# Optimization experiments

Hardware: AMD Instinct MI355X
Metric: run time of the kernel (lower is better)

## Reference

```python
import jax, jax.numpy as jnp
import numpy as np

R = 131072          # total proposals (ROIs)
D = 1024            # input feature dim (ShapeSpec.channels)
NUM_CLASSES = 80    # COCO foreground classes
REID_DIM = 256      # reid_feat_dim
BOX_DIM = 4


def setup_inputs() -> dict:
    key = jax.random.key(0)
    ks = jax.random.split(key, 12)
    x = jax.random.normal(ks[0], (R, D), dtype=jnp.float32)
    # cls_score: Linear(D, num_classes+1), init std=0.01, bias 0
    W_cls = 0.01 * jax.random.normal(ks[1], (NUM_CLASSES + 1, D), dtype=jnp.float32)
    b_cls = jnp.zeros((NUM_CLASSES + 1,), dtype=jnp.float32)
    # bbox_pred: Linear(D, num_classes * 4), init std=0.001, bias 0
    W_bbox = 0.001 * jax.random.normal(ks[2], (NUM_CLASSES * BOX_DIM, D), dtype=jnp.float32)
    b_bbox = jnp.zeros((NUM_CLASSES * BOX_DIM,), dtype=jnp.float32)
    # reid_embed_head: MLP(D, 256, 256, 3) -> Linear(D,256), Linear(256,256), Linear(256,256)
    def lin(k, fan_in, fan_out):
        kw, kb = jax.random.split(k)
        bound = 1.0 / np.sqrt(fan_in)
        W = jax.random.uniform(kw, (fan_out, fan_in), minval=-bound, maxval=bound, dtype=jnp.float32)
        b = jax.random.uniform(kb, (fan_out,), minval=-bound, maxval=bound, dtype=jnp.float32)
        return W, b
    W1, b1 = lin(ks[3], D, REID_DIM)
    W2, b2 = lin(ks[4], REID_DIM, REID_DIM)
    W3, b3 = lin(ks[5], REID_DIM, REID_DIM)
    return {"x": x, "W_cls": W_cls, "b_cls": b_cls, "W_bbox": W_bbox, "b_bbox": b_bbox,
            "W1": W1, "b1": b1, "W2": W2, "b2": b2, "W3": W3, "b3": b3}


def reference(x, W_cls, b_cls, W_bbox, b_bbox, W1, b1, W2, b2, W3, b3):
    # x: [R, D] (already flat; torch forward flattens if dim > 2)
    scores = x @ W_cls.T + b_cls                 # [R, K+1]
    proposal_deltas = x @ W_bbox.T + b_bbox      # [R, K*4]
    # MLP with ReLU on all but last layer
    h = jax.nn.relu(x @ W1.T + b1)               # [R, 256]
    h = jax.nn.relu(h @ W2.T + b2)               # [R, 256]
    embeds = h @ W3.T + b3                       # [R, 256]
    return scores, proposal_deltas, embeds
```

## Files before the change

### kernel.cpp

```cpp
#include <hip/hip_runtime.h>
#include <hip/hip_bf16.h>
#include <stdint.h>

#define R_TOT   131072
#define D_IN    1024
#define N_CLS   81
#define N_BOX   320
#define N_H     256
#define N1_USED 657
#define N1_PAD  672
#define NB_COLS 336

typedef __attribute__((ext_vector_type(8))) short short8;
typedef __attribute__((ext_vector_type(4))) float f32x4;

__device__ __forceinline__ unsigned short f2bf(float f) {
  union { float f; unsigned u; } v; v.f = f;
  unsigned r = v.u + 0x7FFFu + ((v.u >> 16) & 1u);
  return (unsigned short)(r >> 16);
}

__device__ __forceinline__ short8 cvt8(float4 a, float4 b) {
  short8 v;
  v[0] = (short)f2bf(a.x); v[1] = (short)f2bf(a.y);
  v[2] = (short)f2bf(a.z); v[3] = (short)f2bf(a.w);
  v[4] = (short)f2bf(b.x); v[5] = (short)f2bf(b.y);
  v[6] = (short)f2bf(b.z); v[7] = (short)f2bf(b.w);
  return v;
}

__device__ __forceinline__ void async_lds16(void* lds, const void* g) {
  __builtin_amdgcn_global_load_lds(
      (const __attribute__((address_space(1))) unsigned int*)g,
      (__attribute__((address_space(3))) unsigned int*)lds, 16, 0, 0);
}

__global__ void prep_w1(const float* __restrict__ Wc, const float* __restrict__ Wb,
                        const float* __restrict__ W1, unsigned short* __restrict__ Wp)
{
  int idx = blockIdx.x * 256 + threadIdx.x;
  int p   = idx / (N1_PAD * 32);
  int rem = idx % (N1_PAD * 32);
  int n   = rem >> 5;
  int kk  = rem & 31;
  int k   = p * 32 + kk;
  float w = 0.f;
  if (n < N_CLS)               w = Wc[(size_t)n * D_IN + k];
  else if (n < N_CLS + N_BOX)  w = Wb[(size_t)(n - N_CLS) * D_IN + k];
  else if (n < N1_USED)        w = W1[(size_t)(n - (N_CLS + N_BOX)) * D_IN + k];
  Wp[idx] = f2bf(w);
}

__global__ void prep_w23(const float* __restrict__ W2, const float* __restrict__ W3,
                         unsigned short* __restrict__ W2b, unsigned short* __restrict__ W3b)
{
  int idx = blockIdx.x * 256 + threadIdx.x;
  if (idx < 65536) W2b[idx] = f2bf(W2[idx]);
  else             W3b[idx - 65536] = f2bf(W3[idx - 65536]);
}

__global__ __launch_bounds__(448) void g1_kernel(
    const float* __restrict__ x, const unsigned short* __restrict__ Wp,
    const float* __restrict__ b_cls, const float* __restrict__ b_box,
    const float* __restrict__ b1,
    float* __restrict__ scores, float* __restrict__ deltas,
    unsigned short* __restrict__ h1)
{
  __shared__ __attribute__((aligned(16))) unsigned short As[2][64 * 32];

  const int tid  = threadIdx.x;
  const int wave = tid >> 6;
  const int lane = tid & 63;
  const int orig  = blockIdx.x;
  const int work  = (orig & 7) * 512 + (orig >> 3);
  const int m0    = (work >> 1) * 64;
  const int nbase = (work & 1) * NB_COLS;

  const int arow = tid >> 2;
  const int akq  = tid & 3;
  const int awoff = arow * 32 + ((akq ^ ((arow >> 1) & 3)) << 3);

  const int lr = lane & 15;
  const int g2 = (lane >> 4) * 8;

  f32x4 acc[4][3];
#pragma unroll
  for (int i = 0; i < 4; ++i)
#pragma unroll
    for (int j = 0; j < 3; ++j)
      acc[i][j] = (f32x4){0.f, 0.f, 0.f, 0.f};

  const unsigned short* bptr = Wp + (size_t)(nbase + wave * 48 + lr) * 32 + g2;
  const size_t BSTEP = (size_t)N1_PAD * 32;

  if (tid < 256) {
    const float* s = x + (size_t)(m0 + arow) * D_IN + akq * 8;
    float4 f0 = *(const float4*)s;
    float4 f1 = *(const float4*)(s + 4);
    *(short8*)&As[0][awoff] = cvt8(f0, f1);
  }
  short8 bCur0 = *(const short8*)(bptr);
  short8 bCur1 = *(const short8*)(bptr + 512);
  short8 bCur2 = *(const short8*)(bptr + 1024);
  bptr += BSTEP;
  asm volatile("s_waitcnt lgkmcnt(0)" ::: "memory");
  __builtin_amdgcn_sched_barrier(0);
  __builtin_amdgcn_s_barrier();

#pragma unroll 2
  for (int kp = 0; kp < 32; ++kp) {
    const int cur = kp & 1;

    float4 f0, f1;
    if (kp < 31 && tid < 256) {
      const float* s = x + (size_t)(m0 + arow) * D_IN + (size_t)(kp + 1) * 32 + akq * 8;
      f0 = *(const float4*)s;
      f1 = *(const float4*)(s + 4);
    }
    short8 bn0, bn1, bn2;
    if (kp < 31) {
      bn0 = *(const short8*)(bptr);
      bn1 = *(const short8*)(bptr + 512);
      bn2 = *(const short8*)(bptr + 1024);
      bptr += BSTEP;
    }

#pragma unroll
    for (int mi = 0; mi < 4; ++mi) {
      const int r  = mi * 16 + lr;
      const int sl = (g2 >> 3) ^ ((r >> 1) & 3);
      short8 af = *(const short8*)&As[cur][r * 32 + (sl << 3)];
      acc[mi][0] = __builtin_amdgcn_mfma_f32_16x16x32_bf16(af, bCur0, acc[mi][0], 0, 0, 0);
      acc[mi][1] = __builtin_amdgcn_mfma_f32_16x16x32_bf16(af, bCur1, acc[mi][1], 0, 0, 0);
      acc[mi][2] = __builtin_amdgcn_mfma_f32_16x16x32_bf16(af, bCur2, acc[mi][2], 0, 0, 0);
    }

    if (kp < 31 && tid < 256)
      *(short8*)&As[cur ^ 1][awoff] = cvt8(f0, f1);

    if (kp < 31) { bCur0 = bn0; bCur1 = bn1; bCur2 = bn2; }

    asm volatile("s_waitcnt lgkmcnt(0)" ::: "memory");
    __builtin_amdgcn_sched_barrier(0);
    __builtin_amdgcn_s_barrier();
  }

  const int rbase = m0 + ((lane >> 4) << 2);
#pragma unroll
  for (int mi = 0; mi < 4; ++mi) {
#pragma unroll
    for (int ni = 0; ni < 3; ++ni) {
      int n = nbase + wave * 48 + ni * 16 + lr;
      if (n >= N1_USED) continue;
      if (n < N_CLS) {
        float bb = b_cls[n];
#pragma unroll
        for (int j = 0; j < 4; ++j) {
          int r = rbase + mi * 16 + j;
          scores[(size_t)r * N_CLS + n] = acc[mi][ni][j] + bb;
        }
      } else if (n < N_CLS + N_BOX) {
        int nb = n - N_CLS;
        float bb = b_box[nb];
#pragma unroll
        for (int j = 0; j < 4; ++j) {
          int r = rbase + mi * 16 + j;
          deltas[(size_t)r * N_BOX + nb] = acc[mi][ni][j] + bb;
        }
      } else {
        int nh = n - (N_CLS + N_BOX);
        float bb = b1[nh];
#pragma unroll
        for (int j = 0; j < 4; ++j) {
          int r = rbase + mi * 16 + j;
          float h = acc[mi][ni][j] + bb;
          h1[(size_t)r * N_H + nh] = f2bf(fmaxf(h, 0.f));
        }
      }
    }
  }
}

__device__ __forceinline__ void g23_stage(unsigned short* Asb, unsigned short* Bsb,
    const unsigned short* __restrict__ A, const unsigned short* __restrict__ Bw,
    int m0, int kp, int tid)
{
  {
    int row = tid >> 2, kq = tid & 3;
    async_lds16((char*)Asb + tid * 16,
                (const char*)(A + (size_t)(m0 + row) * N_H + (size_t)kp * 32 + kq * 8));
  }
#pragma unroll
  for (int i = 0; i < 2; ++i) {
    int chunk = tid + i * 512;
    int row = chunk >> 2, kq = chunk & 3;
    async_lds16((char*)Bsb + chunk * 16,
                (const char*)(Bw + (size_t)row * N_H + (size_t)kp * 32 + kq * 8));
  }
}

template <int RELU, int OUT_BF16>
__global__ __launch_bounds__(512, 1) void g23_kernel(
    const unsigned short* __restrict__ A, const unsigned short* __restrict__ Bw,
    const float* __restrict__ bias, void* __restrict__ outv)
{
  __shared__ __attribute__((aligned(16))) unsigned short As[2][128 * 32];
  __shared__ __attribute__((aligned(16))) unsigned short Bs[2][256 * 32];
  const int tid  = threadIdx.x;
  const int wave = tid >> 6, lane = tid & 63;
  const int wm = wave >> 2, wn = wave & 3;
  const int m0 = blockIdx.x * 128;

  f32x4 acc[4][4];
#pragma unroll
  for (int i = 0; i < 4; ++i)
#pragma unroll
    for (int j = 0; j < 4; ++j)
      acc[i][j] = (f32x4){0.f, 0.f, 0.f, 0.f};

  g23_stage(&As[0][0], &Bs[0][0], A, Bw, m0, 0, tid);
  __syncthreads();

  const int lr = lane & 15;
  const int lk = (lane >> 4) * 8;

  for (int kp = 0; kp < 8; ++kp) {
    const int cur = kp & 1, nxt = cur ^ 1;
    if (kp < 7) g23_stage(&As[nxt][0], &Bs[nxt][0], A, Bw, m0, kp + 1, tid);

    short8 af[4], bfr[4];
#pragma unroll
    for (int mi = 0; mi < 4; ++mi)
      af[mi] = *(const short8*)&As[cur][(wm * 64 + mi * 16 + lr) * 32 + lk];
#pragma unroll
    for (int ni = 0; ni < 4; ++ni)
      bfr[ni] = *(const short8*)&Bs[cur][(wn * 64 + ni * 16 + lr) * 32 + lk];
#pragma unroll
    for (int mi = 0; mi < 4; ++mi)
#pragma unroll
      for (int ni = 0; ni < 4; ++ni)
        acc[mi][ni] = __builtin_amdgcn_mfma_f32_16x16x32_bf16(af[mi], bfr[ni], acc[mi][ni], 0, 0, 0);
    __syncthreads();
  }

#pragma unroll
  for (int mi = 0; mi < 4; ++mi) {
#pragma unroll
    for (int ni = 0; ni < 4; ++ni) {
      int n = wn * 64 + ni * 16 + lr;
      float bb = bias[n];
#pragma unroll
      for (int j = 0; j < 4; ++j) {
        int r = m0 + wm * 64 + mi * 16 + ((lane >> 4) << 2) + j;
        float v = acc[mi][ni][j] + bb;
        if (RELU) v = fmaxf(v, 0.f);
        if (OUT_BF16) ((unsigned short*)outv)[(size_t)r * N_H + n] = f2bf(v);
        else          ((float*)outv)[(size_t)r * N_H + n] = v;
      }
    }
  }
}

extern "C" void kernel_launch(void* const* d_in, const int* in_sizes, int n_in,
                              void* d_out, int out_size, void* d_ws, size_t ws_size,
                              hipStream_t stream)
{
  const float* x     = (const float*)d_in[0];
  const float* W_cls = (const float*)d_in[1];
  const float* b_cls = (const float*)d_in[2];
  const float* W_box = (const float*)d_in[3];
  const float* b_box = (const float*)d_in[4];
  const float* W1    = (const float*)d_in[5];
  const float* b1    = (const float*)d_in[6];
  const float* W2    = (const float*)d_in[7];
  const float* b2    = (const float*)d_in[8];
  const float* W3    = (const float*)d_in[9];
  const float* b3    = (const float*)d_in[10];

  float* scores = (float*)d_out;
  float* deltas = scores + (size_t)R_TOT * N_CLS;
  float* embeds = deltas + (size_t)R_TOT * N_BOX;

  char* ws = (char*)d_ws;
  unsigned short* Wp  = (unsigned short*)ws;
  unsigned short* W2b = (unsigned short*)(ws + 1376256);
  unsigned short* W3b = (unsigned short*)(ws + 1376256 + 131072);
  unsigned short* h   = (unsigned short*)(ws + 1638400);

  hipLaunchKernelGGL(prep_w1, dim3(2688), dim3(256), 0, stream, W_cls, W_box, W1, Wp);
  hipLaunchKernelGGL(prep_w23, dim3(512), dim3(256), 0, stream, W2, W3, W2b, W3b);
  hipLaunchKernelGGL(g1_kernel, dim3(4096), dim3(448), 0, stream,
                     x, Wp, b_cls, b_box, b1, scores, deltas, h);
  hipLaunchKernelGGL((g23_kernel<1, 1>), dim3(R_TOT / 128), dim3(512), 0, stream,
                     h, W2b, b2, (void*)h);
  hipLaunchKernelGGL((g23_kernel<0, 0>), dim3(R_TOT / 128), dim3(512), 0, stream,
                     h, W3b, b3, (void*)embeds);
}
```

Baseline: 462.1 us.

## Stage half-K A tiles in LDS to cut per-step barriers in g1 GEMM

Replaces the double-buffered 64x32 A tile, which needed a barrier every K step, with a 64x512 bf16 LDS tile loaded twice per block. All 448 threads cooperatively convert x to bf16 with an XOR swizzle, so the inner loop runs 16 steps without synchronisation. It also sets a minimum of 4 blocks per CU in launch_bounds. In exchange, the global loads of x no longer overlap the MFMA work, and LDS use grows to 64KB per block. That LDS size may limit how many blocks fit on a CU.

```diff
diff --git a/kernel.cpp b/kernel.cpp
--- a/kernel.cpp
+++ b/kernel.cpp
@@ -59,14 +59,14 @@
   else             W3b[idx - 65536] = f2bf(W3[idx - 65536]);
 }
 
-__global__ __launch_bounds__(448) void g1_kernel(
+__global__ __launch_bounds__(448, 4) void g1_kernel(
     const float* __restrict__ x, const unsigned short* __restrict__ Wp,
     const float* __restrict__ b_cls, const float* __restrict__ b_box,
     const float* __restrict__ b1,
     float* __restrict__ scores, float* __restrict__ deltas,
     unsigned short* __restrict__ h1)
 {
-  __shared__ __attribute__((aligned(16))) unsigned short As[2][64 * 32];
+  __shared__ __attribute__((aligned(16))) unsigned short As[64 * 512];
 
   const int tid  = threadIdx.x;
   const int wave = tid >> 6;
@@ -76,12 +76,9 @@
   const int m0    = (work >> 1) * 64;
   const int nbase = (work & 1) * NB_COLS;
 
-  const int arow = tid >> 2;
-  const int akq  = tid & 3;
-  const int awoff = arow * 32 + ((akq ^ ((arow >> 1) & 3)) << 3);
-
-  const int lr = lane & 15;
-  const int g2 = (lane >> 4) * 8;
+  const int lr  = lane & 15;
+  const int hig = lane >> 4;
+  const int g2  = hig * 8;
 
   f32x4 acc[4][3];
 #pragma unroll
@@ -93,30 +90,35 @@
   const unsigned short* bptr = Wp + (size_t)(nbase + wave * 48 + lr) * 32 + g2;
   const size_t BSTEP = (size_t)N1_PAD * 32;
 
-  if (tid < 256) {
-    const float* s = x + (size_t)(m0 + arow) * D_IN + akq * 8;
-    float4 f0 = *(const float4*)s;
-    float4 f1 = *(const float4*)(s + 4);
-    *(short8*)&As[0][awoff] = cvt8(f0, f1);
-  }
   short8 bCur0 = *(const short8*)(bptr);
   short8 bCur1 = *(const short8*)(bptr + 512);
   short8 bCur2 = *(const short8*)(bptr + 1024);
   bptr += BSTEP;
-  asm volatile("s_waitcnt lgkmcnt(0)" ::: "memory");
-  __builtin_amdgcn_sched_barrier(0);
-  __builtin_amdgcn_s_barrier();
 
 #pragma unroll 2
   for (int kp = 0; kp < 32; ++kp) {
-    const int cur = kp & 1;
-
-    float4 f0, f1;
-    if (kp < 31 && tid < 256) {
-      const float* s = x + (size_t)(m0 + arow) * D_IN + (size_t)(kp + 1) * 32 + akq * 8;
-      f0 = *(const float4*)s;
-      f1 = *(const float4*)(s + 4);
-    }
+    if ((kp & 15) == 0) {
+      const int c0 = (kp >> 4) * 512;
+      if (kp) __syncthreads();
+#pragma unroll 3
+      for (int i = 0; i < 9; ++i) {
+        int idx = tid + i * 448;
+        int row = idx >> 6, s = idx & 63;
+        const float* src = x + (size_t)(m0 + row) * D_IN + c0 + s * 8;
+        float4 f0 = *(const float4*)src;
+        float4 f1 = *(const float4*)(src + 4);
+        *(short8*)&As[row * 512 + ((s ^ (row & 7)) << 3)] = cvt8(f0, f1);
+      }
+      if (tid < 64) {
+        int s = tid;
+        const float* src = x + (size_t)(m0 + 63) * D_IN + c0 + s * 8;
+        float4 f0 = *(const float4*)src;
+        float4 f1 = *(const float4*)(src + 4);
+        *(short8*)&As[63 * 512 + ((s ^ 7) << 3)] = cvt8(f0, f1);
+      }
+      __syncthreads();
+    }
+
     short8 bn0, bn1, bn2;
     if (kp < 31) {
       bn0 = *(const short8*)(bptr);
@@ -125,27 +127,22 @@
       bptr += BSTEP;
     }
 
+    const int kk = kp & 15;
+    const int sb = kk * 4 + hig;
 #pragma unroll
     for (int mi = 0; mi < 4; ++mi) {
       const int r  = mi * 16 + lr;
-      const int sl = (g2 >> 3) ^ ((r >> 1) & 3);
-      short8 af = *(const short8*)&As[cur][r * 32 + (sl << 3)];
+      const int sl = sb ^ (r & 7);
+      short8 af = *(const short8*)&As[r * 512 + (sl << 3)];
       acc[mi][0] = __builtin_amdgcn_mfma_f32_16x16x32_bf16(af, bCur0, acc[mi][0], 0, 0, 0);
       acc[mi][1] = __builtin_amdgcn_mfma_f32_16x16x32_bf16(af, bCur1, acc[mi][1], 0, 0, 0);
       acc[mi][2] = __builtin_amdgcn_mfma_f32_16x16x32_bf16(af, bCur2, acc[mi][2], 0, 0, 0);
     }
 
-    if (kp < 31 && tid < 256)
-      *(short8*)&As[cur ^ 1][awoff] = cvt8(f0, f1);
-
     if (kp < 31) { bCur0 = bn0; bCur1 = bn1; bCur2 = bn2; }
-
-    asm volatile("s_waitcnt lgkmcnt(0)" ::: "memory");
-    __builtin_amdgcn_sched_barrier(0);
-    __builtin_amdgcn_s_barrier();
-  }
-
-  const int rbase = m0 + ((lane >> 4) << 2);
+  }
+
+  const int rbase = m0 + (hig << 2);
 #pragma unroll
   for (int mi = 0; mi < 4; ++mi) {
 #pragma unroll
```

Measured after the change: 441.1 us. 1.05x faster.
